# Kernel optimization log

Hardware: AMD Instinct MI355X
Metric: run time of the kernel (lower is better)

The kernel has to match this reference:

```python
import jax, jax.numpy as jnp
import numpy as np

# Model config (matches init_kwargs)
D_MODEL = 1536
NUM_HEADS = 16
QUERY_GROUPS = 4
HEAD_DIM = D_MODEL // NUM_HEADS  # 96
HEADS_PER_GROUP = NUM_HEADS // QUERY_GROUPS
ROPE_THETA = 10000.0
B, T, GH, GW = 2, 16, 16, 16
S = GH * GW  # spatial patches per frame
QKV_OUT = NUM_HEADS * HEAD_DIM + 2 * QUERY_GROUPS * HEAD_DIM  # 2304


def setup_inputs() -> dict:
    key = jax.random.key(0)
    k1, k2, k3 = jax.random.split(key, 3)
    x = jax.random.normal(k1, (B, T, S, D_MODEL), dtype=jnp.float32)
    padding_mask = jnp.ones((B * T, S), dtype=jnp.int32)
    # nn.Linear weights stored as [out, in]; y = x @ W.T
    w_qkv = jax.random.normal(k2, (QKV_OUT, D_MODEL), dtype=jnp.float32) * (1.0 / np.sqrt(D_MODEL))
    w_o = jax.random.normal(k3, (D_MODEL, D_MODEL), dtype=jnp.float32) * (1.0 / np.sqrt(D_MODEL))
    return {"x": x, "padding_mask": padding_mask, "w_qkv": w_qkv, "w_o": w_o}


def _rot_half(seg, cos, sin):
    # seg: [..., d]; half-split rotary rotation
    d = seg.shape[-1] // 2
    x1, x2 = seg[..., :d], seg[..., d:]
    return jnp.concatenate([x1 * cos - x2 * sin, x1 * sin + x2 * cos], axis=-1)


def _cos_sin(pos, seg_dim):
    # pos: [L] -> cos/sin [L, seg_dim//2]
    inv_freq = 1.0 / (ROPE_THETA ** (jnp.arange(seg_dim // 2, dtype=jnp.float32) * 2.0 / seg_dim))
    ang = pos.astype(jnp.float32)[:, None] * inv_freq[None, :]
    return jnp.cos(ang), jnp.sin(ang)


def _apply_rope3d(x):
    # x: [B*T, S, heads, HEAD_DIM]; head_dim split equally over (t, h, w) axes
    seg = HEAD_DIM // 3  # 32
    t_pos = jnp.tile(jnp.arange(T), B)            # [B*T] temporal index per attention-batch row
    h_pos = jnp.repeat(jnp.arange(GH), GW)        # [S]
    w_pos = jnp.tile(jnp.arange(GW), GH)          # [S]
    ct, st = _cos_sin(t_pos, seg)  # [B*T, seg/2]
    ch, sh = _cos_sin(h_pos, seg)  # [S, seg/2]
    cw, sw = _cos_sin(w_pos, seg)
    xt = _rot_half(x[..., :seg], ct[:, None, None, :], st[:, None, None, :])
    xh = _rot_half(x[..., seg:2 * seg], ch[None, :, None, :], sh[None, :, None, :])
    xw = _rot_half(x[..., 2 * seg:], cw[None, :, None, :], sw[None, :, None, :])
    return jnp.concatenate([xt, xh, xw], axis=-1)


def reference(x, padding_mask, w_qkv, w_o):
    # Spatial attention mode: [B, T, S, D] -> [B*T, S, D]
    xs = x.reshape(B * T, S, D_MODEL)
    qkv = jnp.einsum('bsd,od->bso', xs, w_qkv)  # [B*T, S, QKV_OUT]
    q_end = NUM_HEADS * HEAD_DIM
    k_end = q_end + QUERY_GROUPS * HEAD_DIM
    q = qkv[..., :q_end].reshape(B * T, S, NUM_HEADS, HEAD_DIM)
    k = qkv[..., q_end:k_end].reshape(B * T, S, QUERY_GROUPS, HEAD_DIM)
    v = qkv[..., k_end:].reshape(B * T, S, QUERY_GROUPS, HEAD_DIM)
    # RoPE3D on q and k
    q = _apply_rope3d(q)
    k = _apply_rope3d(k)
    # GQA: extend kv heads to num_heads (repeat_interleave)
    k = jnp.repeat(k, HEADS_PER_GROUP, axis=2)  # [B*T, S, NUM_HEADS, HEAD_DIM]
    v = jnp.repeat(v, HEADS_PER_GROUP, axis=2)
    scale = 1.0 / np.sqrt(HEAD_DIM)
    scores = jnp.einsum('bqhd,bkhd->bhqk', q, k) * scale  # [B*T, H, S, S]
    mask = (padding_mask != 0)[:, None, None, :]  # [B*T, 1, 1, S], True = attend
    scores = jnp.where(mask, scores, jnp.float32(-1e9))
    probs = jax.nn.softmax(scores, axis=-1)
    attn = jnp.einsum('bhqk,bkhd->bqhd', probs, v).reshape(B * T, S, D_MODEL)
    out = jnp.einsum('bsd,od->bso', attn, w_o)
    return out.reshape(B, T, S, D_MODEL)
```

## Files before the change

kernel.cpp:

```cpp
#include <hip/hip_runtime.h>
#include <hip/hip_bf16.h>
#include <stdint.h>

typedef __attribute__((ext_vector_type(8))) short short8;
typedef __attribute__((ext_vector_type(4))) float f32x4;
typedef __attribute__((ext_vector_type(4))) float f4;
typedef __attribute__((ext_vector_type(4))) short s4;

typedef __attribute__((address_space(1))) const void gvoid_t;
typedef __attribute__((address_space(3))) void lvoid_t;

__device__ __forceinline__ void gload_lds16(const void* g, void* l) {
  __builtin_amdgcn_global_load_lds((gvoid_t*)g, (lvoid_t*)l, 16, 0, 0);
}

__device__ __forceinline__ ushort f2b(float f) {
  union { float f; uint32_t u; } v; v.f = f;
  return (ushort)((v.u + 0x7fffu + ((v.u >> 16) & 1u)) >> 16);
}
__device__ __forceinline__ float b2f(ushort b) {
  union { uint32_t u; float f; } v; v.u = ((uint32_t)b) << 16;
  return v.f;
}

template <int N> __device__ __forceinline__ void wait_vmcnt();
template <> __device__ __forceinline__ void wait_vmcnt<0>() { asm volatile("s_waitcnt vmcnt(0)" ::: "memory"); }

__device__ __forceinline__ void wait_lgkm0() {
  asm volatile("s_waitcnt lgkmcnt(0)" ::: "memory");
  __builtin_amdgcn_sched_barrier(0);
}
__device__ __forceinline__ void barrier_fence() {
  asm volatile("s_barrier" ::: "memory");
}

__global__ void prep_kernel(const float* __restrict__ x, const float* __restrict__ wq,
                            const float* __restrict__ wo,
                            ushort* __restrict__ Xb, ushort* __restrict__ Wq,
                            ushort* __restrict__ Wo, float2* __restrict__ tab) {
  int b = blockIdx.x, tid = threadIdx.x;
  const float* in; ushort* out; int i;
  if (b < 12288)      { in = x;  out = Xb; i = b * 256 + tid; }
  else if (b < 15744) { in = wq; out = Wq; i = (b - 12288) * 256 + tid; }
  else if (b < 18048) { in = wo; out = Wo; i = (b - 15744) * 256 + tid; }
  else {
    int pos = tid >> 4, fi = tid & 15;
    float inv_freq = __expf(-(float)fi * 0.5756462732485115f);
    float ang = (float)pos * inv_freq;
    float sn, c;
    __sincosf(ang, &sn, &c);
    tab[tid] = make_float2(c, sn);
    return;
  }
  f4 v = ((const f4*)in)[i];
  s4 o;
  o.x = (short)f2b(v.x); o.y = (short)f2b(v.y);
  o.z = (short)f2b(v.z); o.w = (short)f2b(v.w);
  ((s4*)out)[i] = o;
}

template <int BN, typename OutT>
__global__ __launch_bounds__(512, 2) void gemm6(const ushort* __restrict__ A,
                                                const ushort* __restrict__ B,
                                                OutT* __restrict__ C,
                                                int N, int K) {
  constexpr int NF = BN / 32;
  constexpr int RB = BN / 2;
  constexpr int ABUF = 256 * 64;
  constexpr int BBUF = BN * 64;
  constexpr uint ABYTE = ABUF * 2;
  constexpr uint BBYTE = BBUF * 2;
  constexpr int BRND = BN / 64;
  constexpr int BTW = (BN % 64) / 8;

  __shared__ ushort As[2 * ABUF];
  __shared__ ushort Bs[2 * BBUF];

  const int tid = threadIdx.x;
  const int l = tid & 63, w = tid >> 6;
  const int wr = w >> 1, wc = w & 1;
  const int r16 = l & 15, kh = l >> 4;
  const int sc = (l & 7) ^ (l >> 3);
  const int srow = w * 8 + (l >> 3);

  const int xcd = blockIdx.x & 7;
  const int ii = blockIdx.x >> 3;
  const int bm = xcd * 4 + (ii & 3);
  const int bn = ii >> 2;
  const ushort* Ag = A + (size_t)bm * 256 * K;
  const ushort* Bg = B + (size_t)bn * BN * K;
  const int NT = K >> 6;

  const char* AsR = (const char*)As;
  const char* BsR = (const char*)Bs;
  const uint khsw = ((uint)kh * 16) ^ ((uint)(r16 & 7) * 16);
  const uint PA = (uint)(wr * 64 + r16) * 128 + khsw;
  const uint PB = (uint)(wc * RB + r16) * 128 + khsw;

  const ushort* ga[4];
  const ushort* gb[BRND];
  const ushort* gbt = nullptr;
#pragma unroll
  for (int i = 0; i < 4; ++i) ga[i] = Ag + (size_t)(i * 64 + srow) * K + sc * 8;
#pragma unroll
  for (int i = 0; i < BRND; ++i) gb[i] = Bg + (size_t)(i * 64 + srow) * K + sc * 8;
  if constexpr (BTW > 0) gbt = Bg + (size_t)(BRND * 64 + srow) * K + sc * 8;

#pragma unroll
  for (int i = 0; i < 4; ++i) gload_lds16(ga[i], As + i * 4096 + w * 512);
#pragma unroll
  for (int i = 0; i < BRND; ++i) gload_lds16(gb[i], Bs + i * 4096 + w * 512);
  if constexpr (BTW > 0) { if (w < BTW) gload_lds16(gbt, Bs + BRND * 4096 + w * 512); }
#pragma unroll
  for (int i = 0; i < 4; ++i) ga[i] += 64;
#pragma unroll
  for (int i = 0; i < BRND; ++i) gb[i] += 64;
  if constexpr (BTW > 0) gbt += 64;
  wait_vmcnt<0>();
  barrier_fence();

  f32x4 acc[4][NF] = {};
  short8 afr[4], bfr[NF];

  for (int u = 0; u < NT; ++u) {
    const int cur = u & 1;
    const uint aoff = cur ? ABYTE : 0u;
    const uint boff = cur ? BBYTE : 0u;
    ushort* An = As + (cur ^ 1) * ABUF;
    ushort* Bn = Bs + (cur ^ 1) * BBUF;
    const bool st = (u + 1 < NT);

    {
      const uint pa = PA + aoff, pb = PB + boff;
#pragma unroll
      for (int m = 0; m < 4; ++m) afr[m] = *(const short8*)(AsR + pa + m * 2048);
#pragma unroll
      for (int n = 0; n < NF; ++n) bfr[n] = *(const short8*)(BsR + pb + n * 2048);
    }
    if (st) {
#pragma unroll
      for (int i = 0; i < 4; ++i) gload_lds16(ga[i], An + i * 4096 + w * 512);
    }
    wait_lgkm0();
    __builtin_amdgcn_s_setprio(1);
#pragma unroll
    for (int m = 0; m < 4; ++m)
#pragma unroll
      for (int n = 0; n < NF; ++n)
        acc[m][n] = __builtin_amdgcn_mfma_f32_16x16x32_bf16(afr[m], bfr[n], acc[m][n], 0, 0, 0);
    __builtin_amdgcn_s_setprio(0);

    {
      const uint pa = (PA ^ 64u) + aoff, pb = (PB ^ 64u) + boff;
#pragma unroll
      for (int m = 0; m < 4; ++m) afr[m] = *(const short8*)(AsR + pa + m * 2048);
#pragma unroll
      for (int n = 0; n < NF; ++n) bfr[n] = *(const short8*)(BsR + pb + n * 2048);
    }
    if (st) {
#pragma unroll
      for (int i = 0; i < BRND; ++i) gload_lds16(gb[i], Bn + i * 4096 + w * 512);
      if constexpr (BTW > 0) { if (w < BTW) gload_lds16(gbt, Bn + BRND * 4096 + w * 512); }
    }
    wait_lgkm0();
    __builtin_amdgcn_s_setprio(1);
#pragma unroll
    for (int m = 0; m < 4; ++m)
#pragma unroll
      for (int n = 0; n < NF; ++n)
        acc[m][n] = __builtin_amdgcn_mfma_f32_16x16x32_bf16(afr[m], bfr[n], acc[m][n], 0, 0, 0);
    __builtin_amdgcn_s_setprio(0);

#pragma unroll
    for (int i = 0; i < 4; ++i) ga[i] += 64;
#pragma unroll
    for (int i = 0; i < BRND; ++i) gb[i] += 64;
    if constexpr (BTW > 0) gbt += 64;
    wait_vmcnt<0>();
    barrier_fence();
  }

  const int rowb = bm * 256 + wr * 64;
  const int colb = bn * BN + wc * RB;
#pragma unroll
  for (int m = 0; m < 4; ++m)
#pragma unroll
    for (int n = 0; n < NF; ++n)
#pragma unroll
      for (int r = 0; r < 4; ++r) {
        int row = rowb + m * 16 + kh * 4 + r;
        int col = colb + n * 16 + r16;
        float val = acc[m][n][r];
        if constexpr (sizeof(OutT) == 2) C[(size_t)row * N + col] = f2b(val);
        else                             C[(size_t)row * N + col] = val;
      }
}

__device__ __forceinline__ short8 shfl_xor32(short8 v) {
  union { short8 s; int i[4]; } a, b;
  a.s = v;
#pragma unroll
  for (int q = 0; q < 4; ++q) b.i[q] = __shfl_xor(a.i[q], 32, 64);
  return b.s;
}
__device__ __forceinline__ short8 rope_frag(short8 v, int pos, int kh, const float2* Tb) {
  short8 p = shfl_xor32(v);
  const float sgn = (kh < 2) ? -1.0f : 1.0f;
  const int ib = pos * 16 + (kh & 1) * 8;
  short8 o;
#pragma unroll
  for (int j = 0; j < 8; ++j) {
    float2 cs = Tb[ib + j];
    o[j] = (short)f2b(b2f((ushort)v[j]) * cs.x + sgn * b2f((ushort)p[j]) * cs.y);
  }
  return o;
}

__global__ __launch_bounds__(512, 1) void attn3_kernel(
    const ushort* __restrict__ QKV,
    const int* __restrict__ mask,
    const float2* __restrict__ Tab,
    ushort* __restrict__ Out) {
  __shared__ ushort Ks[256 * 104];
  __shared__ ushort Vs[96 * 264];
  __shared__ ushort Ps[8][16 * 136];
  __shared__ float Mb[256];
  __shared__ float2 Tb[256];

  const int b = blockIdx.x;
  const int qt = b & 1;
  const int g = (b >> 1) & 3;
  const int bt = b >> 3;
  const int t = threadIdx.x;
  const int l = t & 63, w = t >> 6;
  const int r16 = l & 15, kh = l >> 4;
  const int h = g * 4 + (w >> 1);
  const int qc = w & 1;
  const int t0 = bt & 15;

  if (t < 256) { Tb[t] = Tab[t]; Mb[t] = mask[bt * 256 + t] ? 0.0f : -1.0e9f; }
  __syncthreads();

  {
    const int r = t >> 1, ch = t & 1;
    const ushort* src = QKV + (size_t)(bt * 256 + r) * 2304 + 1536 + g * 96;
    const int p1 = r >> 4, p2 = r & 15;
    if (ch == 0) {
      short8 v0 = *(const short8*)(src + 0);
      short8 v1 = *(const short8*)(src + 8);
      short8 v2 = *(const short8*)(src + 16);
      short8 v3 = *(const short8*)(src + 24);
      short8 o0, o1, o2, o3;
#pragma unroll
      for (int j = 0; j < 8; ++j) {
        float2 ca = Tb[t0 * 16 + j], cb = Tb[t0 * 16 + 8 + j];
        float x1a = b2f((ushort)v0[j]), x2a = b2f((ushort)v2[j]);
        float x1b = b2f((ushort)v1[j]), x2b = b2f((ushort)v3[j]);
        o0[j] = (short)f2b(x1a * ca.x - x2a * ca.y);
        o1[j] = (short)f2b(x1b * cb.x - x2b * cb.y);
        o2[j] = (short)f2b(x1a * ca.y + x2a * ca.x);
        o3[j] = (short)f2b(x1b * cb.y + x2b * cb.x);
      }
      *(short8*)(&Ks[r * 104 + 0])  = o0;
      *(short8*)(&Ks[r * 104 + 8])  = o1;
      *(short8*)(&Ks[r * 104 + 16]) = o2;
      *(short8*)(&Ks[r * 104 + 24]) = o3;
      v0 = *(const short8*)(src + 32);
      v1 = *(const short8*)(src + 40);
      v2 = *(const short8*)(src + 48);
      v3 = *(const short8*)(src + 56);
#pragma unroll
      for (int j = 0; j < 8; ++j) {
        float2 ca = Tb[p1 * 16 + j], cb = Tb[p1 * 16 + 8 + j];
        float x1a = b2f((ushort)v0[j]), x2a = b2f((ushort)v2[j]);
        float x1b = b2f((ushort)v1[j]), x2b = b2f((ushort)v3[j]);
        o0[j] = (short)f2b(x1a * ca.x - x2a * ca.y);
        o1[j] = (short)f2b(x1b * cb.x - x2b * cb.y);
        o2[j] = (short)f2b(x1a * ca.y + x2a * ca.x);
        o3[j] = (short)f2b(x1b * cb.y + x2b * cb.x);
      }
      *(short8*)(&Ks[r * 104 + 32]) = o0;
      *(short8*)(&Ks[r * 104 + 40]) = o1;
      *(short8*)(&Ks[r * 104 + 48]) = o2;
      *(short8*)(&Ks[r * 104 + 56]) = o3;
    } else {
      short8 v0 = *(const short8*)(src + 64);
      short8 v1 = *(const short8*)(src + 72);
      short8 v2 = *(const short8*)(src + 80);
      short8 v3 = *(const short8*)(src + 88);
      short8 o0, o1, o2, o3;
#pragma unroll
      for (int j = 0; j < 8; ++j) {
        float2 ca = Tb[p2 * 16 + j], cb = Tb[p2 * 16 + 8 + j];
        float x1a = b2f((ushort)v0[j]), x2a = b2f((ushort)v2[j]);
        float x1b = b2f((ushort)v1[j]), x2b = b2f((ushort)v3[j]);
        o0[j] = (short)f2b(x1a * ca.x - x2a * ca.y);
        o1[j] = (short)f2b(x1b * cb.x - x2b * cb.y);
        o2[j] = (short)f2b(x1a * ca.y + x2a * ca.x);
        o3[j] = (short)f2b(x1b * cb.y + x2b * cb.x);
      }
      *(short8*)(&Ks[r * 104 + 64]) = o0;
      *(short8*)(&Ks[r * 104 + 72]) = o1;
      *(short8*)(&Ks[r * 104 + 80]) = o2;
      *(short8*)(&Ks[r * 104 + 88]) = o3;
    }
  }

#pragma unroll
  for (int i = 0; i < 6; ++i) {
    int c = t + i * 512;
    int s = c / 12, dq = c - s * 12;
    short8 vv = *(const short8*)(QKV + (size_t)(bt * 256 + s) * 2304 + 1920 + g * 96 + dq * 8);
#pragma unroll
    for (int j = 0; j < 8; ++j)
      Vs[(dq * 8 + j) * 264 + s] = (ushort)vv[j];
  }
  __syncthreads();

  const ushort* Qp = QKV + (size_t)(bt * 256 + qt * 128 + qc * 64) * 2304 + h * 96;
  ushort* Pw = &Ps[w][0];
  const float scale = 0.10206207261596575f;

#pragma unroll
  for (int mp = 0; mp < 2; ++mp) {
    const int qb = mp * 32;
    const int p1A = qt * 8 + qc * 4 + mp * 2;
    const int p1B = p1A + 1;

    short8 qfA[3], qfB[3];
    {
      short8 rA0 = *(const short8*)(Qp + (size_t)(qb + r16) * 2304 + 0 + kh * 8);
      short8 rA1 = *(const short8*)(Qp + (size_t)(qb + r16) * 2304 + 32 + kh * 8);
      short8 rA2 = *(const short8*)(Qp + (size_t)(qb + r16) * 2304 + 64 + kh * 8);
      short8 rB0 = *(const short8*)(Qp + (size_t)(qb + 16 + r16) * 2304 + 0 + kh * 8);
      short8 rB1 = *(const short8*)(Qp + (size_t)(qb + 16 + r16) * 2304 + 32 + kh * 8);
      short8 rB2 = *(const short8*)(Qp + (size_t)(qb + 16 + r16) * 2304 + 64 + kh * 8);
      qfA[0] = rope_frag(rA0, t0, kh, Tb);
      qfA[1] = rope_frag(rA1, p1A, kh, Tb);
      qfA[2] = rope_frag(rA2, r16, kh, Tb);
      qfB[0] = rope_frag(rB0, t0, kh, Tb);
      qfB[1] = rope_frag(rB1, p1B, kh, Tb);
      qfB[2] = rope_frag(rB2, r16, kh, Tb);
    }

    f32x4 scA[16] = {}, scB[16] = {};
#pragma unroll
    for (int f = 0; f < 16; ++f) {
#pragma unroll
      for (int kc = 0; kc < 3; ++kc) {
        short8 kf = *(const short8*)(&Ks[(f * 16 + r16) * 104 + kc * 32 + kh * 8]);
        scA[f] = __builtin_amdgcn_mfma_f32_16x16x32_bf16(qfA[kc], kf, scA[f], 0, 0, 0);
        scB[f] = __builtin_amdgcn_mfma_f32_16x16x32_bf16(qfB[kc], kf, scB[f], 0, 0, 0);
      }
    }

#pragma unroll
    for (int f = 0; f < 16; ++f) {
      float mb = Mb[f * 16 + r16];
#pragma unroll
      for (int r = 0; r < 4; ++r) {
        scA[f][r] = scA[f][r] * scale + mb;
        scB[f][r] = scB[f][r] * scale + mb;
      }
    }

    float invA[4], invB[4];
#pragma unroll
    for (int reg = 0; reg < 4; ++reg) {
      float mxA = -3.0e38f, mxB = -3.0e38f;
#pragma unroll
      for (int f = 0; f < 16; ++f) { mxA = fmaxf(mxA, scA[f][reg]); mxB = fmaxf(mxB, scB[f][reg]); }
      for (int o = 8; o >= 1; o >>= 1) { mxA = fmaxf(mxA, __shfl_xor(mxA, o, 64)); mxB = fmaxf(mxB, __shfl_xor(mxB, o, 64)); }
      float smA = 0.f, smB = 0.f;
#pragma unroll
      for (int f = 0; f < 16; ++f) {
        float pA = __expf(scA[f][reg] - mxA);
        float pB = __expf(scB[f][reg] - mxB);
        scA[f][reg] = pA; scB[f][reg] = pB;
        smA += pA; smB += pB;
      }
      for (int o = 8; o >= 1; o >>= 1) { smA += __shfl_xor(smA, o, 64); smB += __shfl_xor(smB, o, 64); }
      invA[reg] = 1.0f / smA;
      invB[reg] = 1.0f / smB;
    }

    short8 pfA[8], pfB[8];
#pragma unroll
    for (int ck = 0; ck < 2; ++ck) {
#pragma unroll
      for (int f = 0; f < 8; ++f)
#pragma unroll
        for (int reg = 0; reg < 4; ++reg)
          Pw[(kh * 4 + reg) * 136 + f * 16 + r16] = f2b(scA[ck * 8 + f][reg]);
#pragma unroll
      for (int kc = 0; kc < 4; ++kc)
        pfA[ck * 4 + kc] = *(const short8*)(&Pw[r16 * 136 + kc * 32 + kh * 8]);
    }
#pragma unroll
    for (int ck = 0; ck < 2; ++ck) {
#pragma unroll
      for (int f = 0; f < 8; ++f)
#pragma unroll
        for (int reg = 0; reg < 4; ++reg)
          Pw[(kh * 4 + reg) * 136 + f * 16 + r16] = f2b(scB[ck * 8 + f][reg]);
#pragma unroll
      for (int kc = 0; kc < 4; ++kc)
        pfB[ck * 4 + kc] = *(const short8*)(&Pw[r16 * 136 + kc * 32 + kh * 8]);
    }

    f32x4 oA[6] = {}, oB[6] = {};
#pragma unroll
    for (int dt = 0; dt < 6; ++dt) {
#pragma unroll
      for (int kc = 0; kc < 8; ++kc) {
        short8 vf = *(const short8*)(&Vs[(dt * 16 + r16) * 264 + kc * 32 + kh * 8]);
        oA[dt] = __builtin_amdgcn_mfma_f32_16x16x32_bf16(pfA[kc], vf, oA[dt], 0, 0, 0);
        oB[dt] = __builtin_amdgcn_mfma_f32_16x16x32_bf16(pfB[kc], vf, oB[dt], 0, 0, 0);
      }
    }

    const int rbase = bt * 256 + qt * 128 + qc * 64 + qb;
#pragma unroll
    for (int dt = 0; dt < 6; ++dt)
#pragma unroll
      for (int reg = 0; reg < 4; ++reg) {
        int col = h * 96 + dt * 16 + r16;
        Out[(size_t)(rbase + kh * 4 + reg) * 1536 + col]      = f2b(oA[dt][reg] * invA[reg]);
        Out[(size_t)(rbase + 16 + kh * 4 + reg) * 1536 + col] = f2b(oB[dt][reg] * invB[reg]);
      }
  }
}

extern "C" void kernel_launch(void* const* d_in, const int* in_sizes, int n_in,
                              void* d_out, int out_size, void* d_ws, size_t ws_size,
                              hipStream_t stream) {
  const float* x     = (const float*)d_in[0];
  const int* pmask   = (const int*)d_in[1];
  const float* w_qkv = (const float*)d_in[2];
  const float* w_o   = (const float*)d_in[3];
  float* out = (float*)d_out;

  char* ws = (char*)d_ws;
  ushort* Xb  = (ushort*)(ws + 0);
  ushort* Wq  = (ushort*)(ws + 25165824);
  ushort* Wo  = (ushort*)(ws + 32243712);
  ushort* QKV = (ushort*)(ws + 36962304);
  float2* Tab = (float2*)(ws + 74711040);
  ushort* Attn = Xb;

  prep_kernel<<<18049, 256, 0, stream>>>(x, w_qkv, w_o, Xb, Wq, Wo, Tab);

  gemm6<288, ushort><<<256, 512, 0, stream>>>(Xb, Wq, QKV, 2304, 1536);

  attn3_kernel<<<256, 512, 0, stream>>>(QKV, pmask, Tab, Attn);

  gemm6<192, float><<<256, 512, 0, stream>>>(Attn, Wo, out, 1536, 1536);
}
```

Measured before the change: 147.0 us.

## Use 4-wave GEMM blocks with 128-row warp tiles and compile-time K

The GEMM kernel moves from 8 waves per 512-thread block to 4 waves per 256-thread block. Each wave now computes 128 rows instead of 64, doubling its A fragments and accumulators, and K and N become template constants. The aim is to reuse each B fragment across more MFMAs and to cut per-wave LDS read traffic and address arithmetic. In exchange, register pressure roughly doubles, the launch bound drops to one block per CU, and fewer waves are available to hide latency. The global-to-LDS load loops are also restructured for the smaller thread count.

Result: slower. 370.4 us (+152.0%).

```diff
diff --git a/kernel.cpp b/kernel.cpp
--- a/kernel.cpp
+++ b/kernel.cpp
@@ -59,19 +59,19 @@
   ((s4*)out)[i] = o;
 }
 
-template <int BN, typename OutT>
-__global__ __launch_bounds__(512, 2) void gemm6(const ushort* __restrict__ A,
-                                                const ushort* __restrict__ B,
-                                                OutT* __restrict__ C,
-                                                int N, int K) {
+template <int BN, int KC, typename OutT>
+__global__ __launch_bounds__(256, 1) void gemm11(const ushort* __restrict__ A,
+                                                 const ushort* __restrict__ B,
+                                                 OutT* __restrict__ C) {
   constexpr int NF = BN / 32;
   constexpr int RB = BN / 2;
   constexpr int ABUF = 256 * 64;
   constexpr int BBUF = BN * 64;
   constexpr uint ABYTE = ABUF * 2;
   constexpr uint BBYTE = BBUF * 2;
-  constexpr int BRND = BN / 64;
-  constexpr int BTW = (BN % 64) / 8;
+  constexpr int ARND = 8;
+  constexpr int BRND = BN / 32;
+  constexpr int NT = KC >> 6;
 
   __shared__ ushort As[2 * ABUF];
   __shared__ ushort Bs[2 * BBUF];
@@ -87,40 +87,28 @@
   const int ii = blockIdx.x >> 3;
   const int bm = xcd * 4 + (ii & 3);
   const int bn = ii >> 2;
-  const ushort* Ag = A + (size_t)bm * 256 * K;
-  const ushort* Bg = B + (size_t)bn * BN * K;
-  const int NT = K >> 6;
+  const ushort* Ag = A + (size_t)bm * 256 * KC;
+  const ushort* Bg = B + (size_t)bn * BN * KC;
 
   const char* AsR = (const char*)As;
   const char* BsR = (const char*)Bs;
   const uint khsw = ((uint)kh * 16) ^ ((uint)(r16 & 7) * 16);
-  const uint PA = (uint)(wr * 64 + r16) * 128 + khsw;
+  const uint PA = (uint)(wr * 128 + r16) * 128 + khsw;
   const uint PB = (uint)(wc * RB + r16) * 128 + khsw;
 
-  const ushort* ga[4];
-  const ushort* gb[BRND];
-  const ushort* gbt = nullptr;
-#pragma unroll
-  for (int i = 0; i < 4; ++i) ga[i] = Ag + (size_t)(i * 64 + srow) * K + sc * 8;
-#pragma unroll
-  for (int i = 0; i < BRND; ++i) gb[i] = Bg + (size_t)(i * 64 + srow) * K + sc * 8;
-  if constexpr (BTW > 0) gbt = Bg + (size_t)(BRND * 64 + srow) * K + sc * 8;
-
-#pragma unroll
-  for (int i = 0; i < 4; ++i) gload_lds16(ga[i], As + i * 4096 + w * 512);
-#pragma unroll
-  for (int i = 0; i < BRND; ++i) gload_lds16(gb[i], Bs + i * 4096 + w * 512);
-  if constexpr (BTW > 0) { if (w < BTW) gload_lds16(gbt, Bs + BRND * 4096 + w * 512); }
-#pragma unroll
-  for (int i = 0; i < 4; ++i) ga[i] += 64;
-#pragma unroll
-  for (int i = 0; i < BRND; ++i) gb[i] += 64;
-  if constexpr (BTW > 0) gbt += 64;
+  const ushort* gA = Ag + (size_t)srow * KC + sc * 8;
+  const ushort* gB = Bg + (size_t)srow * KC + sc * 8;
+
+#pragma unroll
+  for (int i = 0; i < ARND; ++i) gload_lds16(gA + (size_t)(i * 32) * KC, As + i * 2048 + w * 512);
+#pragma unroll
+  for (int i = 0; i < BRND; ++i) gload_lds16(gB + (size_t)(i * 32) * KC, Bs + i * 2048 + w * 512);
+  gA += 64; gB += 64;
   wait_vmcnt<0>();
   barrier_fence();
 
-  f32x4 acc[4][NF] = {};
-  short8 afr[4], bfr[NF];
+  f32x4 acc[8][NF] = {};
+  short8 afr[8], bfr[NF];
 
   for (int u = 0; u < NT; ++u) {
     const int cur = u & 1;
@@ -133,18 +121,18 @@
     {
       const uint pa = PA + aoff, pb = PB + boff;
 #pragma unroll
-      for (int m = 0; m < 4; ++m) afr[m] = *(const short8*)(AsR + pa + m * 2048);
+      for (int m = 0; m < 8; ++m) afr[m] = *(const short8*)(AsR + pa + m * 2048);
 #pragma unroll
       for (int n = 0; n < NF; ++n) bfr[n] = *(const short8*)(BsR + pb + n * 2048);
     }
     if (st) {
 #pragma unroll
-      for (int i = 0; i < 4; ++i) gload_lds16(ga[i], An + i * 4096 + w * 512);
+      for (int i = 0; i < ARND; ++i) gload_lds16(gA + (size_t)(i * 32) * KC, An + i * 2048 + w * 512);
     }
     wait_lgkm0();
     __builtin_amdgcn_s_setprio(1);
 #pragma unroll
-    for (int m = 0; m < 4; ++m)
+    for (int m = 0; m < 8; ++m)
 #pragma unroll
       for (int n = 0; n < NF; ++n)
         acc[m][n] = __builtin_amdgcn_mfma_f32_16x16x32_bf16(afr[m], bfr[n], acc[m][n], 0, 0, 0);
@@ -153,37 +141,32 @@
     {
       const uint pa = (PA ^ 64u) + aoff, pb = (PB ^ 64u) + boff;
 #pragma unroll
-      for (int m = 0; m < 4; ++m) afr[m] = *(const short8*)(AsR + pa + m * 2048);
+      for (int m = 0; m < 8; ++m) afr[m] = *(const short8*)(AsR + pa + m * 2048);
 #pragma unroll
       for (int n = 0; n < NF; ++n) bfr[n] = *(const short8*)(BsR + pb + n * 2048);
     }
     if (st) {
 #pragma unroll
-      for (int i = 0; i < BRND; ++i) gload_lds16(gb[i], Bn + i * 4096 + w * 512);
-      if constexpr (BTW > 0) { if (w < BTW) gload_lds16(gbt, Bn + BRND * 4096 + w * 512); }
+      for (int i = 0; i < BRND; ++i) gload_lds16(gB + (size_t)(i * 32) * KC, Bn + i * 2048 + w * 512);
     }
     wait_lgkm0();
     __builtin_amdgcn_s_setprio(1);
 #pragma unroll
-    for (int m = 0; m < 4; ++m)
+    for (int m = 0; m < 8; ++m)
 #pragma unroll
       for (int n = 0; n < NF; ++n)
         acc[m][n] = __builtin_amdgcn_mfma_f32_16x16x32_bf16(afr[m], bfr[n], acc[m][n], 0, 0, 0);
     __builtin_amdgcn_s_setprio(0);
 
-#pragma unroll
-    for (int i = 0; i < 4; ++i) ga[i] += 64;
-#pragma unroll
-    for (int i = 0; i < BRND; ++i) gb[i] += 64;
-    if constexpr (BTW > 0) gbt += 64;
+    gA += 64; gB += 64;
     wait_vmcnt<0>();
     barrier_fence();
   }
 
-  const int rowb = bm * 256 + wr * 64;
+  const int rowb = bm * 256 + wr * 128;
   const int colb = bn * BN + wc * RB;
 #pragma unroll
-  for (int m = 0; m < 4; ++m)
+  for (int m = 0; m < 8; ++m)
 #pragma unroll
     for (int n = 0; n < NF; ++n)
 #pragma unroll
@@ -191,8 +174,8 @@
         int row = rowb + m * 16 + kh * 4 + r;
         int col = colb + n * 16 + r16;
         float val = acc[m][n][r];
-        if constexpr (sizeof(OutT) == 2) C[(size_t)row * N + col] = f2b(val);
-        else                             C[(size_t)row * N + col] = val;
+        if constexpr (sizeof(OutT) == 2) C[(size_t)row * (BN * 8) + col] = f2b(val);
+        else                             C[(size_t)row * (BN * 8) + col] = val;
       }
 }
 
@@ -450,9 +433,9 @@
 
   prep_kernel<<<18049, 256, 0, stream>>>(x, w_qkv, w_o, Xb, Wq, Wo, Tab);
 
-  gemm6<288, ushort><<<256, 512, 0, stream>>>(Xb, Wq, QKV, 2304, 1536);
+  gemm11<288, 1536, ushort><<<256, 256, 0, stream>>>(Xb, Wq, QKV);
 
   attn3_kernel<<<256, 512, 0, stream>>>(QKV, pmask, Tab, Attn);
 
-  gemm6<192, float><<<256, 512, 0, stream>>>(Attn, Wo, out, 1536, 1536);
-}
+  gemm11<192, 1536, float><<<256, 256, 0, stream>>>(Attn, Wo, out);
+}
```

## Use smaller-tile 256-thread GEMM with split double-buffer loads for output projection

Applied to the files above, without the earlier changes.

Adds a gemm12 kernel with 128-row tiles, 256 threads, two blocks per CU and compile-time K, and uses it for the output projection instead of gemm6. The A and B prefetches for the next K tile are interleaved between the two MFMA half-steps, with setprio raised around the MFMA bursts. A grid of 512 blocks mapped by XCD is meant to improve occupancy and latency hiding on this GEMM. The cost is less data reuse per block, since A is reloaded for each N tile.

New measurement: 147.5 us. No clear change (+0.3%).

```diff
diff --git a/kernel.cpp b/kernel.cpp
--- a/kernel.cpp
+++ b/kernel.cpp
@@ -196,6 +196,126 @@
       }
 }
 
+template <int BN, int KC, typename OutT>
+__global__ __launch_bounds__(256, 2) void gemm12(const ushort* __restrict__ A,
+                                                 const ushort* __restrict__ B,
+                                                 OutT* __restrict__ C) {
+  constexpr int NF = BN / 32;
+  constexpr int RB = BN / 2;
+  constexpr int ABUF = 128 * 64;
+  constexpr int BBUF = BN * 64;
+  constexpr uint ABYTE = ABUF * 2;
+  constexpr uint BBYTE = BBUF * 2;
+  constexpr int ARND = 4;
+  constexpr int BRND = BN / 32;
+  constexpr int NT = KC >> 6;
+
+  __shared__ ushort As[2 * ABUF];
+  __shared__ ushort Bs[2 * BBUF];
+
+  const int tid = threadIdx.x;
+  const int l = tid & 63, w = tid >> 6;
+  const int wr = w >> 1, wc = w & 1;
+  const int r16 = l & 15, kh = l >> 4;
+  const int sc = (l & 7) ^ (l >> 3);
+  const int srow = w * 8 + (l >> 3);
+
+  const int xcd = blockIdx.x & 7;
+  const int ii = blockIdx.x >> 3;
+  const int bm = xcd * 8 + (ii & 7);
+  const int bn = ii >> 3;
+  const ushort* Ag = A + (size_t)bm * 128 * KC;
+  const ushort* Bg = B + (size_t)bn * BN * KC;
+
+  const char* AsR = (const char*)As;
+  const char* BsR = (const char*)Bs;
+  const uint khsw = ((uint)kh * 16) ^ ((uint)(r16 & 7) * 16);
+  const uint PA = (uint)(wr * 64 + r16) * 128 + khsw;
+  const uint PB = (uint)(wc * RB + r16) * 128 + khsw;
+
+  const ushort* gA = Ag + (size_t)srow * KC + sc * 8;
+  const ushort* gB = Bg + (size_t)srow * KC + sc * 8;
+
+#pragma unroll
+  for (int i = 0; i < ARND; ++i) gload_lds16(gA + (size_t)(i * 32) * KC, As + i * 2048 + w * 512);
+#pragma unroll
+  for (int i = 0; i < BRND; ++i) gload_lds16(gB + (size_t)(i * 32) * KC, Bs + i * 2048 + w * 512);
+  gA += 64; gB += 64;
+  wait_vmcnt<0>();
+  barrier_fence();
+
+  f32x4 acc[4][NF] = {};
+  short8 afr[4], bfr[NF];
+
+  for (int u = 0; u < NT; ++u) {
+    const int cur = u & 1;
+    const uint aoff = cur ? ABYTE : 0u;
+    const uint boff = cur ? BBYTE : 0u;
+    ushort* An = As + (cur ^ 1) * ABUF;
+    ushort* Bn = Bs + (cur ^ 1) * BBUF;
+    const bool st = (u + 1 < NT);
+
+    {
+      const uint pa = PA + aoff, pb = PB + boff;
+#pragma unroll
+      for (int m = 0; m < 4; ++m) afr[m] = *(const short8*)(AsR + pa + m * 2048);
+#pragma unroll
+      for (int n = 0; n < NF; ++n) bfr[n] = *(const short8*)(BsR + pb + n * 2048);
+    }
+    if (st) {
+#pragma unroll
+      for (int i = 0; i < ARND; ++i) gload_lds16(gA + (size_t)(i * 32) * KC, An + i * 2048 + w * 512);
+    }
+    wait_lgkm0();
+    __builtin_amdgcn_s_setprio(1);
+#pragma unroll
+    for (int m = 0; m < 4; ++m)
+#pragma unroll
+      for (int n = 0; n < NF; ++n)
+        acc[m][n] = __builtin_amdgcn_mfma_f32_16x16x32_bf16(afr[m], bfr[n], acc[m][n], 0, 0, 0);
+    __builtin_amdgcn_s_setprio(0);
+
+    {
+      const uint pa = (PA ^ 64u) + aoff, pb = (PB ^ 64u) + boff;
+#pragma unroll
+      for (int m = 0; m < 4; ++m) afr[m] = *(const short8*)(AsR + pa + m * 2048);
+#pragma unroll
+      for (int n = 0; n < NF; ++n) bfr[n] = *(const short8*)(BsR + pb + n * 2048);
+    }
+    if (st) {
+#pragma unroll
+      for (int i = 0; i < BRND; ++i) gload_lds16(gB + (size_t)(i * 32) * KC, Bn + i * 2048 + w * 512);
+    }
+    wait_lgkm0();
+    __builtin_amdgcn_s_setprio(1);
+#pragma unroll
+    for (int m = 0; m < 4; ++m)
+#pragma unroll
+      for (int n = 0; n < NF; ++n)
+        acc[m][n] = __builtin_amdgcn_mfma_f32_16x16x32_bf16(afr[m], bfr[n], acc[m][n], 0, 0, 0);
+    __builtin_amdgcn_s_setprio(0);
+
+    gA += 64; gB += 64;
+    wait_vmcnt<0>();
+    barrier_fence();
+  }
+
+  const int rowb = bm * 128 + wr * 64;
+  const int colb = bn * BN + wc * RB;
+#pragma unroll
+  for (int m = 0; m < 4; ++m)
+#pragma unroll
+    for (int n = 0; n < NF; ++n)
+#pragma unroll
+      for (int r = 0; r < 4; ++r) {
+        int row = rowb + m * 16 + kh * 4 + r;
+        int col = colb + n * 16 + r16;
+        float val = acc[m][n][r];
+        if constexpr (sizeof(OutT) == 2) C[(size_t)row * (BN * 8) + col] = f2b(val);
+        else                             C[(size_t)row * (BN * 8) + col] = val;
+      }
+}
+
 __device__ __forceinline__ short8 shfl_xor32(short8 v) {
   union { short8 s; int i[4]; } a, b;
   a.s = v;
@@ -454,5 +574,5 @@
 
   attn3_kernel<<<256, 512, 0, stream>>>(QKV, pmask, Tab, Attn);
 
-  gemm6<192, float><<<256, 512, 0, stream>>>(Attn, Wo, out, 1536, 1536);
-}
+  gemm12<192, 1536, float><<<512, 256, 0, stream>>>(Attn, Wo, out);
+}
```
